# Performance work log

Hardware: AMD Instinct MI355X
Metric: run time of the kernel (lower is better)

## Reference

```python
import jax, jax.numpy as jnp
import numpy as np

N, E, R, H, FDIM, OUT = 50000, 800000, 12, 128, 1582, 2
Q = H // 4  # 32
SLOPE = 0.01  # LeakyReLU default negative slope


def leaky(x):
    return jnp.where(x > 0, x, SLOPE * x)


def rgcn(x, src, dst, etype, W, root, bias):
    # Per-relation mean aggregation of neighbor features, then linear transform
    # (PyG RGCNConv default aggr='mean'). Linear => transform-then-mean is equal.
    # count of edges of each (relation, dst) pair
    seg = etype * N + dst
    cnt = jnp.zeros((R * N,), x.dtype).at[seg].add(1.0)
    norm = 1.0 / jnp.maximum(cnt[seg], 1.0)          # [E]
    xw = jnp.einsum('nh,rhd->nrd', x, W)             # [N,R,H] per-relation transform
    msg = xw[src, etype] * norm[:, None]             # [E,H] gather + normalize
    agg = jax.ops.segment_sum(msg, dst, num_segments=N)  # [N,H] scatter-add
    return agg + x @ root + bias


def setup_inputs() -> dict:
    key = jax.random.key(0)
    ks = jax.random.split(key, 16)
    s = lambda d: 1.0 / np.sqrt(d)
    inp = {
        'feature': jax.random.normal(ks[0], (N, FDIM), jnp.float32),
        'edge_index': jax.random.randint(ks[1], (2, E), 0, N),
        'edge_type': jax.random.randint(ks[2], (E,), 0, R),
        'W_des': jax.random.normal(ks[3], (768, Q), jnp.float32) * s(768),
        'b_des': jnp.zeros((Q,), jnp.float32),
        'W_tweet': jax.random.normal(ks[4], (768, Q), jnp.float32) * s(768),
        'b_tweet': jnp.zeros((Q,), jnp.float32),
        'W_num': jax.random.normal(ks[5], (34, Q), jnp.float32) * s(34),
        'b_num': jnp.zeros((Q,), jnp.float32),
        'W_cat': jax.random.normal(ks[6], (12, Q), jnp.float32) * s(12),
        'b_cat': jnp.zeros((Q,), jnp.float32),
        'W_in': jax.random.normal(ks[7], (H, H), jnp.float32) * s(H),
        'b_in': jnp.zeros((H,), jnp.float32),
        'rgcn_W': jax.random.normal(ks[8], (R, H, H), jnp.float32) * s(H),
        'rgcn_root': jax.random.normal(ks[9], (H, H), jnp.float32) * s(H),
        'rgcn_bias': jnp.zeros((H,), jnp.float32),
        'W_out1': jax.random.normal(ks[10], (H, H), jnp.float32) * s(H),
        'b_out1': jnp.zeros((H,), jnp.float32),
        'W_out2': jax.random.normal(ks[11], (H, OUT), jnp.float32) * s(H),
        'b_out2': jnp.zeros((OUT,), jnp.float32),
    }
    return inp


def reference(feature, edge_index, edge_type, W_des, b_des, W_tweet, b_tweet,
              W_num, b_num, W_cat, b_cat, W_in, b_in, rgcn_W, rgcn_root,
              rgcn_bias, W_out1, b_out1, W_out2, b_out2):
    src, dst = edge_index[0], edge_index[1]
    d = leaky(feature[:, -1536:-768] @ W_des + b_des)
    t = leaky(feature[:, -768:] @ W_tweet + b_tweet)
    num = leaky(feature[:, 12:46] @ W_num + b_num)
    cat = leaky(feature[:, 0:12] @ W_cat + b_cat)
    x = jnp.concatenate((d, t, num, cat), axis=1)       # [N,H]
    x = leaky(x @ W_in + b_in)
    x = rgcn(x, src, dst, edge_type, rgcn_W, rgcn_root, rgcn_bias)
    # dropout: identity in eval mode (deterministic reference)
    x = rgcn(x, src, dst, edge_type, rgcn_W, rgcn_root, rgcn_bias)
    x = leaky(x @ W_out1 + b_out1)
    return x @ W_out2 + b_out2
```

## Files before the change

### kernel.cpp

```cpp
#include <hip/hip_runtime.h>
#include <stdint.h>

#define NN 50000
#define NE 800000
#define NR 12
#define NRX 13
#define NH 128
#define NF 1582
#define NSEG (NN * NR)
#define MT 3125
#define MT2 1563
#define SCAN_NB ((NSEG + 255) / 256)
#define KSENC 50
#define CTXW (NRX * 8)

typedef __attribute__((ext_vector_type(8))) short short8;
typedef __attribute__((ext_vector_type(4))) float floatx4;

__device__ __forceinline__ float bf2f(unsigned int u16) {
    union { unsigned int i; float f; } w; w.i = u16 << 16; return w.f;
}
__device__ __forceinline__ unsigned short f2bf(float f) {
    union { float f; unsigned int i; } w; w.f = f;
    unsigned int i = w.i;
    return (unsigned short)((i + 0x7FFFu + ((i >> 16) & 1u)) >> 16);
}
__device__ __forceinline__ float leaky_f(float v) { return v > 0.f ? v : 0.01f * v; }
__device__ __forceinline__ float fast_rcp(float x) {
    float r; asm("v_rcp_f32 %0, %1" : "=v"(r) : "v"(x)); return r;
}

__global__ __launch_bounds__(256) void swz_k(
    const float* __restrict__ src1, int K1,
    const float* __restrict__ src2, int Ktot, int N, int KS,
    unsigned short* __restrict__ dst)
{
    const int idx = blockIdx.x * 256 + threadIdx.x;
    const int total = (N >> 4) * KS * 512;
    if (idx >= total) return;
    const int j = idx & 7;
    const int lane = (idx >> 3) & 63;
    const int cks = idx >> 9;
    const int ks = cks % KS;
    const int ct = cks / KS;
    const int k = ks * 32 + (lane >> 4) * 8 + j;
    const int col = ct * 16 + (lane & 15);
    float v = 0.f;
    if (k < Ktot) v = (k < K1) ? src1[(size_t)k * N + col] : src2[(size_t)(k - K1) * N + col];
    dst[idx] = f2bf(v);
}

__global__ __launch_bounds__(256) void swzxw_k(
    const float* __restrict__ rgW, const float* __restrict__ root,
    unsigned short* __restrict__ dst)
{
    const int idx = blockIdx.x * 256 + threadIdx.x;
    const int total = CTXW * 4 * 512;
    if (idx >= total) return;
    const int j = idx & 7;
    const int lane = (idx >> 3) & 63;
    const int cks = idx >> 9;
    const int ks = cks & 3;
    const int ctg = cks >> 2;
    const int r = ctg >> 3;
    const int ct8 = ctg & 7;
    const int k = ks * 32 + (lane >> 4) * 8 + j;
    const int c = ct8 * 16 + (lane & 15);
    const float v = (r < NR) ? rgW[((size_t)r * NH + k) * NH + c]
                             : root[(size_t)k * NH + c];
    dst[idx] = f2bf(v);
}

__global__ __launch_bounds__(256) void swzenc_k(
    const float* __restrict__ Wdes, const float* __restrict__ Wtw,
    const float* __restrict__ Wnum, const float* __restrict__ Wcat,
    unsigned short* __restrict__ dst)
{
    const int idx = blockIdx.x * 256 + threadIdx.x;
    const int total = 8 * KSENC * 512;
    if (idx >= total) return;
    const int j = idx & 7;
    const int lane = (idx >> 3) & 63;
    const int cks = idx >> 9;
    const int ks = cks % KSENC;
    const int ct = cks / KSENC;
    const int k = ks * 32 + (lane >> 4) * 8 + j;
    const int col = ct * 16 + (lane & 15);
    float v = 0.f;
    if (col < 32) {
        if (k >= 46 && k < 814)   v = Wdes[(size_t)(k - 46) * 32 + col];
    } else if (col < 64) {
        if (k >= 814 && k < 1582) v = Wtw[(size_t)(k - 814) * 32 + (col - 32)];
    } else if (col < 96) {
        if (k >= 12 && k < 46)    v = Wnum[(size_t)(k - 12) * 32 + (col - 64)];
    } else {
        if (k < 12)               v = Wcat[(size_t)k * 32 + (col - 96)];
    }
    dst[idx] = f2bf(v);
}

__global__ __launch_bounds__(128) void packbias_k(
    const float* __restrict__ bdes, const float* __restrict__ btw,
    const float* __restrict__ bnum, const float* __restrict__ bcat,
    float* __restrict__ be)
{
    const int c = threadIdx.x;
    float v;
    if (c < 32) v = bdes[c];
    else if (c < 64) v = btw[c - 32];
    else if (c < 96) v = bnum[c - 64];
    else v = bcat[c - 96];
    be[c] = v;
}

__global__ __launch_bounds__(256) void hist_k(const int* __restrict__ dst,
                                              const int* __restrict__ et,
                                              int* __restrict__ deg)
{
    const int e = blockIdx.x * 256 + threadIdx.x;
    if (e >= NE) return;
    atomicAdd(&deg[dst[e] * NR + et[e]], 1);
}

__global__ __launch_bounds__(256) void scanA_k(const int* __restrict__ deg,
                                               int* __restrict__ offs,
                                               int* __restrict__ part)
{
    __shared__ int lds[256];
    const int i = blockIdx.x * 256 + threadIdx.x;
    const int v = (i < NSEG) ? deg[i] : 0;
    lds[threadIdx.x] = v; __syncthreads();
#pragma unroll
    for (int d = 1; d < 256; d <<= 1) {
        const int t = (threadIdx.x >= d) ? lds[threadIdx.x - d] : 0;
        __syncthreads();
        lds[threadIdx.x] += t;
        __syncthreads();
    }
    if (i < NSEG) offs[i] = lds[threadIdx.x] - v;
    if (threadIdx.x == 255) part[blockIdx.x] = lds[255];
}

__global__ __launch_bounds__(256) void scanB_k(int* __restrict__ part, int nb)
{
    __shared__ int lds[256];
    __shared__ int carry;
    if (threadIdx.x == 0) carry = 0;
    __syncthreads();
    for (int base = 0; base < nb; base += 256) {
        const int i = base + threadIdx.x;
        const int v = (i < nb) ? part[i] : 0;
        lds[threadIdx.x] = v; __syncthreads();
#pragma unroll
        for (int d = 1; d < 256; d <<= 1) {
            const int t = (threadIdx.x >= d) ? lds[threadIdx.x - d] : 0;
            __syncthreads();
            lds[threadIdx.x] += t;
            __syncthreads();
        }
        if (i < nb) part[i] = lds[threadIdx.x] - v + carry;
        __syncthreads();
        if (threadIdx.x == 255) carry += lds[255];
        __syncthreads();
    }
}

__global__ __launch_bounds__(256) void scanC_k(int* __restrict__ offs,
                                               const int* __restrict__ part)
{
    const int i = blockIdx.x * 256 + threadIdx.x;
    if (i < NSEG) offs[i] += part[blockIdx.x];
}

__global__ __launch_bounds__(256) void fill_k(const int* __restrict__ src,
                                              const int* __restrict__ dst,
                                              const int* __restrict__ et,
                                              const int* __restrict__ offs,
                                              const int* __restrict__ deg,
                                              int* __restrict__ cur,
                                              unsigned int* __restrict__ eidx)
{
    const int e = blockIdx.x * 256 + threadIdx.x;
    if (e >= NE) return;
    const int r = et[e];
    const int s = dst[e] * NR + r;
    const int pos = offs[s] + atomicAdd(&cur[s], 1);
    int n = deg[s]; if (n > 4095) n = 4095;
    eidx[pos] = (unsigned int)(src[e] * NRX + r) | ((unsigned int)n << 20);
}

__global__ __launch_bounds__(256) void enc_k(
    const float* __restrict__ feat,
    const unsigned short* __restrict__ Benc, const float* __restrict__ be,
    const unsigned short* __restrict__ Bwin, const float* __restrict__ bin,
    unsigned short* __restrict__ xa)
{
    const int wave = threadIdx.x >> 6, lane = threadIdx.x & 63;
    const int q = lane >> 4, cl = lane & 15;
    int tile = blockIdx.x * 4 + wave;
    if (tile >= MT) tile = MT - 1;
    const int row = tile * 16 + cl;

    const int lo[8] = {1, 1, 25, 25, 0, 0, 0, 0};
    const int hi[8] = {26, 26, 50, 50, 2, 2, 1, 1};

    floatx4 acc[8];
#pragma unroll
    for (int ct = 0; ct < 8; ct++) { floatx4 z = {0.f,0.f,0.f,0.f}; acc[ct] = z; }

    for (int ks = 0; ks < KSENC; ks++) {
        const int kb = ks * 32 + q * 8;
        union { short8 v; unsigned short u[8]; } a;
        const float* ap = feat + (size_t)row * NF + kb;
        if (kb + 7 < NF) {
#pragma unroll
            for (int j = 0; j < 4; j++) {
                const float2 t = *(const float2*)__builtin_assume_aligned(ap + 2 * j, 8);
                a.u[2 * j]     = f2bf(t.x);
                a.u[2 * j + 1] = f2bf(t.y);
            }
        } else {
#pragma unroll
            for (int j = 0; j < 8; j++)
                a.u[j] = ((kb + j) < NF) ? f2bf(ap[j]) : 0;
        }
#pragma unroll
        for (int ct = 0; ct < 8; ct++) {
            if (ks >= lo[ct] && ks < hi[ct]) {
                const short8 b = *(const short8*)(Benc + ((size_t)(ct * KSENC + ks) * 64 + lane) * 8);
                acc[ct] = __builtin_amdgcn_mfma_f32_16x16x32_bf16(a.v, b, acc[ct], 0, 0, 0);
            }
        }
    }

    __shared__ unsigned short lds[4][16][136];
#pragma unroll
    for (int ct = 0; ct < 8; ct++) {
        const int col = ct * 16 + cl;
        const float bv = be[col];
#pragma unroll
        for (int r = 0; r < 4; r++)
            lds[wave][q * 4 + r][col] = f2bf(leaky_f(acc[ct][r] + bv));
    }
    __syncthreads();

    floatx4 acc2[8];
#pragma unroll
    for (int ct = 0; ct < 8; ct++) { floatx4 z = {0.f,0.f,0.f,0.f}; acc2[ct] = z; }
#pragma unroll
    for (int ks2 = 0; ks2 < 4; ks2++) {
        const short8 a2 = *(const short8*)&lds[wave][cl][ks2 * 32 + q * 8];
#pragma unroll
        for (int ct = 0; ct < 8; ct++) {
            const short8 b = *(const short8*)(Bwin + ((size_t)(ct * 4 + ks2) * 64 + lane) * 8);
            acc2[ct] = __builtin_amdgcn_mfma_f32_16x16x32_bf16(a2, b, acc2[ct], 0, 0, 0);
        }
    }
#pragma unroll
    for (int ct = 0; ct < 8; ct++) {
        const int col = ct * 16 + cl;
        const float bv = bin[col];
#pragma unroll
        for (int r = 0; r < 4; r++)
            xa[(size_t)(tile * 16 + q * 4 + r) * NH + col] = f2bf(leaky_f(acc2[ct][r] + bv));
    }
}

__global__ __launch_bounds__(256) void xw_k(
    const unsigned short* __restrict__ xin,
    const unsigned short* __restrict__ Bxw,
    unsigned short* __restrict__ xw)
{
    const int wave = threadIdx.x >> 6, lane = threadIdx.x & 63;
    const int q = lane >> 4, cl = lane & 15;
    const int wid = blockIdx.x * 4 + wave;
    if (wid >= MT2 * NRX) return;
    const int t2 = wid / NRX;
    const int r = wid - t2 * NRX;
    const int ta = t2 * 2;
    const int tb = (ta + 1 < MT) ? ta + 1 : MT - 1;

    floatx4 accA[8], accB[8];
#pragma unroll
    for (int ct = 0; ct < 8; ct++) {
        floatx4 z = {0.f,0.f,0.f,0.f}; accA[ct] = z; accB[ct] = z;
    }
#pragma unroll
    for (int ks = 0; ks < 4; ks++) {
        const short8 aA = *(const short8*)__builtin_assume_aligned(
            xin + (size_t)(ta * 16 + cl) * NH + ks * 32 + q * 8, 16);
        const short8 aB = *(const short8*)__builtin_assume_aligned(
            xin + (size_t)(tb * 16 + cl) * NH + ks * 32 + q * 8, 16);
#pragma unroll
        for (int ct = 0; ct < 8; ct++) {
            const short8 b = *(const short8*)(Bxw + ((size_t)((r * 8 + ct) * 4 + ks) * 64 + lane) * 8);
            accA[ct] = __builtin_amdgcn_mfma_f32_16x16x32_bf16(aA, b, accA[ct], 0, 0, 0);
            accB[ct] = __builtin_amdgcn_mfma_f32_16x16x32_bf16(aB, b, accB[ct], 0, 0, 0);
        }
    }
#pragma unroll
    for (int ct = 0; ct < 8; ct++) {
        const int col = ct * 16 + cl;
#pragma unroll
        for (int rr = 0; rr < 4; rr++) {
            xw[((size_t)(ta * 16 + q * 4 + rr) * NRX + r) * NH + col] = f2bf(accA[ct][rr]);
            xw[((size_t)(tb * 16 + q * 4 + rr) * NRX + r) * NH + col] = f2bf(accB[ct][rr]);
        }
    }
}

#define ACC8(fk, t, w) \
    fk[0] += (w) * bf2f(t.x & 0xFFFFu); fk[1] += (w) * bf2f(t.x >> 16); \
    fk[2] += (w) * bf2f(t.y & 0xFFFFu); fk[3] += (w) * bf2f(t.y >> 16); \
    fk[4] += (w) * bf2f(t.z & 0xFFFFu); fk[5] += (w) * bf2f(t.z >> 16); \
    fk[6] += (w) * bf2f(t.w & 0xFFFFu); fk[7] += (w) * bf2f(t.w >> 16);

__global__ __launch_bounds__(256) void gather_k(
    const unsigned short* __restrict__ xw,
    const unsigned int* __restrict__ eidx,
    const int* __restrict__ offs,
    const float* __restrict__ rbias,
    unsigned short* __restrict__ xout)
{
    const int wave = threadIdx.x >> 6, lane = threadIdx.x & 63;
    const int q = lane >> 4, cl = lane & 15;
    const int tile = blockIdx.x * 4 + wave;
    if (tile >= MT) return;
    const int d = tile * 16 + cl;
    const int beg = offs[d * NR];
    const int end = (d < NN - 1) ? offs[(d + 1) * NR] : NE;

    float f[4][8];
    {
        const unsigned short* xr = xw + ((size_t)d * NRX + NR) * NH + q * 8;
#pragma unroll
        for (int ki = 0; ki < 4; ki++) {
            const uint4 t = *(const uint4*)(xr + ki * 32);
            f[ki][0] = bf2f(t.x & 0xFFFFu); f[ki][1] = bf2f(t.x >> 16);
            f[ki][2] = bf2f(t.y & 0xFFFFu); f[ki][3] = bf2f(t.y >> 16);
            f[ki][4] = bf2f(t.z & 0xFFFFu); f[ki][5] = bf2f(t.z >> 16);
            f[ki][6] = bf2f(t.w & 0xFFFFu); f[ki][7] = bf2f(t.w >> 16);
        }
    }

    unsigned int vnext = (beg < end) ? eidx[beg] : 0u;
    for (int e = beg; e < end; ++e) {
        const unsigned int val = vnext;
        if (e + 1 < end) vnext = eidx[e + 1];
        const float w = fast_rcp((float)(val >> 20));
        const unsigned short* xr = xw + (size_t)(val & 0xFFFFFu) * NH + q * 8;
        const uint4 t0 = *(const uint4*)(xr);
        const uint4 t1 = *(const uint4*)(xr + 32);
        const uint4 t2 = *(const uint4*)(xr + 64);
        const uint4 t3 = *(const uint4*)(xr + 96);
        ACC8(f[0], t0, w); ACC8(f[1], t1, w); ACC8(f[2], t2, w); ACC8(f[3], t3, w);
    }

#pragma unroll
    for (int ki = 0; ki < 4; ki++) {
        union { short8 v; unsigned short u[8]; } o;
#pragma unroll
        for (int m = 0; m < 8; m++)
            o.u[m] = f2bf(f[ki][m] + rbias[ki * 32 + q * 8 + m]);
        *(short8*)(xout + (size_t)d * NH + ki * 32 + q * 8) = o.v;
    }
}

__global__ __launch_bounds__(256) void head_k(
    const unsigned short* __restrict__ xa,
    const unsigned short* __restrict__ Bo1, const float* __restrict__ bo1,
    const float* __restrict__ Wo2, const float* __restrict__ bo2,
    float* __restrict__ out)
{
    const int wave = threadIdx.x >> 6, lane = threadIdx.x & 63;
    const int q = lane >> 4, cl = lane & 15;
    int tile = blockIdx.x * 4 + wave;
    if (tile >= MT) tile = MT - 1;

    floatx4 acc[8];
#pragma unroll
    for (int ct = 0; ct < 8; ct++) { floatx4 z = {0.f,0.f,0.f,0.f}; acc[ct] = z; }
#pragma unroll
    for (int ks = 0; ks < 4; ks++) {
        const short8 a = *(const short8*)__builtin_assume_aligned(
            xa + (size_t)(tile * 16 + cl) * NH + ks * 32 + q * 8, 16);
#pragma unroll
        for (int ct = 0; ct < 8; ct++) {
            const short8 b = *(const short8*)(Bo1 + ((size_t)(ct * 4 + ks) * 64 + lane) * 8);
            acc[ct] = __builtin_amdgcn_mfma_f32_16x16x32_bf16(a, b, acc[ct], 0, 0, 0);
        }
    }
    __shared__ unsigned short lds[4][16][136];
#pragma unroll
    for (int ct = 0; ct < 8; ct++) {
        const int col = ct * 16 + cl;
        const float bv = bo1[col];
#pragma unroll
        for (int r = 0; r < 4; r++)
            lds[wave][q * 4 + r][col] = f2bf(leaky_f(acc[ct][r] + bv));
    }
    __syncthreads();

    if (lane < 32) {
        const int row = lane >> 1, o = lane & 1;
        float s = bo2[o];
        for (int k = 0; k < NH; k++)
            s += bf2f(lds[wave][row][k]) * Wo2[k * 2 + o];
        out[(size_t)(tile * 16 + row) * 2 + o] = s;
    }
}

extern "C" void kernel_launch(void* const* d_in, const int* in_sizes, int n_in,
                              void* d_out, int out_size, void* d_ws, size_t ws_size,
                              hipStream_t stream)
{
    const float* feat = (const float*)d_in[0];
    const int* ei   = (const int*)d_in[1];
    const int* et   = (const int*)d_in[2];
    const float* Wdes = (const float*)d_in[3];
    const float* bdes = (const float*)d_in[4];
    const float* Wtw  = (const float*)d_in[5];
    const float* btw  = (const float*)d_in[6];
    const float* Wnum = (const float*)d_in[7];
    const float* bnum = (const float*)d_in[8];
    const float* Wcat = (const float*)d_in[9];
    const float* bcat = (const float*)d_in[10];
    const float* Win  = (const float*)d_in[11];
    const float* bin  = (const float*)d_in[12];
    const float* rgW  = (const float*)d_in[13];
    const float* root = (const float*)d_in[14];
    const float* rbias= (const float*)d_in[15];
    const float* Wo1  = (const float*)d_in[16];
    const float* bo1  = (const float*)d_in[17];
    const float* Wo2  = (const float*)d_in[18];
    const float* bo2  = (const float*)d_in[19];
    const int* srcp = ei;
    const int* dstp = ei + NE;

    char* p = (char*)d_ws;
    auto alloc = [&](size_t bytes) { char* r = p; p += (bytes + 255) & ~(size_t)255; return r; };
    unsigned short* xa = (unsigned short*)alloc((size_t)NN * NH * 2);
    unsigned short* xb = (unsigned short*)alloc((size_t)NN * NH * 2);
    int* deg  = (int*)alloc((size_t)NSEG * 4);
    int* offs = (int*)alloc((size_t)NSEG * 4);
    int* cur  = (int*)alloc((size_t)NSEG * 4);
    int* part = (int*)alloc((size_t)(SCAN_NB + 8) * 4);
    unsigned int* eidx = (unsigned int*)alloc((size_t)NE * 4);
    unsigned short* Benc = (unsigned short*)alloc((size_t)8 * KSENC * 512 * 2);
    unsigned short* sWin = (unsigned short*)alloc((size_t)8 * 4 * 512 * 2);
    unsigned short* Bxw  = (unsigned short*)alloc((size_t)CTXW * 4 * 512 * 2);
    unsigned short* sWo1 = (unsigned short*)alloc((size_t)8 * 4 * 512 * 2);
    float* be = (float*)alloc(128 * 4);
    unsigned short* xwbuf = (unsigned short*)alloc((size_t)NN * NRX * NH * 2);

    const int GB = (MT + 3) / 4;
    const int GBXW = (MT2 * NRX + 3) / 4;

    hipMemsetAsync(deg, 0, (size_t)NSEG * 4, stream);
    hipMemsetAsync(cur, 0, (size_t)NSEG * 4, stream);
    hist_k<<<(NE + 255) / 256, 256, 0, stream>>>(dstp, et, deg);
    scanA_k<<<SCAN_NB, 256, 0, stream>>>(deg, offs, part);
    scanB_k<<<1, 256, 0, stream>>>(part, SCAN_NB);
    scanC_k<<<SCAN_NB, 256, 0, stream>>>(offs, part);
    fill_k<<<(NE + 255) / 256, 256, 0, stream>>>(srcp, dstp, et, offs, deg, cur, eidx);

    swzenc_k<<<(8 * KSENC * 512 + 255) / 256, 256, 0, stream>>>(Wdes, Wtw, Wnum, Wcat, Benc);
    packbias_k<<<1, 128, 0, stream>>>(bdes, btw, bnum, bcat, be);
    swz_k<<<(8 * 4 * 512 + 255) / 256, 256, 0, stream>>>(Win, 128, Win, 128, 128, 4, sWin);
    swzxw_k<<<(CTXW * 4 * 512 + 255) / 256, 256, 0, stream>>>(rgW, root, Bxw);
    swz_k<<<(8 * 4 * 512 + 255) / 256, 256, 0, stream>>>(Wo1, 128, Wo1, 128, 128, 4, sWo1);

    enc_k<<<GB, 256, 0, stream>>>(feat, Benc, be, sWin, bin, xa);
    xw_k<<<GBXW, 256, 0, stream>>>(xa, Bxw, xwbuf);
    gather_k<<<GB, 256, 0, stream>>>(xwbuf, eidx, offs, rbias, xb);
    xw_k<<<GBXW, 256, 0, stream>>>(xb, Bxw, xwbuf);
    gather_k<<<GB, 256, 0, stream>>>(xwbuf, eidx, offs, rbias, xa);
    head_k<<<GB, 256, 0, stream>>>(xa, sWo1, bo1, Wo2, bo2, (float*)d_out);
}
```

Baseline: 863.4 us.

## Stage xw output through LDS for coalesced stores; split gather across two waves per tile

The xw kernel now writes each wave's bf16 result tile into shared memory and then emits 16-byte row-contiguous stores, replacing the scattered 2-byte column stores. The out-of-range waves are clamped instead of returning so every thread reaches the block barrier. The gather kernel assigns two waves per 16-node tile, each covering half the feature columns. It also unrolls the edge loop by two so more independent gathers are in flight. This doubles the index and offset reads per node and adds LDS traffic and a block-wide sync in xw.

```diff
diff --git a/kernel.cpp b/kernel.cpp
--- a/kernel.cpp
+++ b/kernel.cpp
@@ -273,8 +273,9 @@
 {
     const int wave = threadIdx.x >> 6, lane = threadIdx.x & 63;
     const int q = lane >> 4, cl = lane & 15;
-    const int wid = blockIdx.x * 4 + wave;
-    if (wid >= MT2 * NRX) return;
+    int wid = blockIdx.x * 4 + wave;
+    if (wid >= MT2 * NRX) wid = MT2 * NRX - 1;
+    __shared__ unsigned short tl[4][2][16][136];
     const int t2 = wid / NRX;
     const int r = wid - t2 * NRX;
     const int ta = t2 * 2;
@@ -303,17 +304,32 @@
         const int col = ct * 16 + cl;
 #pragma unroll
         for (int rr = 0; rr < 4; rr++) {
-            xw[((size_t)(ta * 16 + q * 4 + rr) * NRX + r) * NH + col] = f2bf(accA[ct][rr]);
-            xw[((size_t)(tb * 16 + q * 4 + rr) * NRX + r) * NH + col] = f2bf(accB[ct][rr]);
-        }
-    }
-}
-
-#define ACC8(fk, t, w) \
-    fk[0] += (w) * bf2f(t.x & 0xFFFFu); fk[1] += (w) * bf2f(t.x >> 16); \
-    fk[2] += (w) * bf2f(t.y & 0xFFFFu); fk[3] += (w) * bf2f(t.y >> 16); \
-    fk[4] += (w) * bf2f(t.z & 0xFFFFu); fk[5] += (w) * bf2f(t.z >> 16); \
-    fk[6] += (w) * bf2f(t.w & 0xFFFFu); fk[7] += (w) * bf2f(t.w >> 16);
+            tl[wave][0][q * 4 + rr][col] = f2bf(accA[ct][rr]);
+            tl[wave][1][q * 4 + rr][col] = f2bf(accB[ct][rr]);
+        }
+    }
+    __syncthreads();
+#pragma unroll
+    for (int i = 0; i < 4; i++) {
+        const int row = i * 4 + q;
+        const short8 vA = *(const short8*)&tl[wave][0][row][cl * 8];
+        const short8 vB = *(const short8*)&tl[wave][1][row][cl * 8];
+        *(short8*)(xw + ((size_t)(ta * 16 + row) * NRX + r) * NH + cl * 8) = vA;
+        *(short8*)(xw + ((size_t)(tb * 16 + row) * NRX + r) * NH + cl * 8) = vB;
+    }
+}
+
+#define ACC8(fk, tv, wv) \
+    fk[0] += (wv) * bf2f((tv).x & 0xFFFFu); fk[1] += (wv) * bf2f((tv).x >> 16); \
+    fk[2] += (wv) * bf2f((tv).y & 0xFFFFu); fk[3] += (wv) * bf2f((tv).y >> 16); \
+    fk[4] += (wv) * bf2f((tv).z & 0xFFFFu); fk[5] += (wv) * bf2f((tv).z >> 16); \
+    fk[6] += (wv) * bf2f((tv).w & 0xFFFFu); fk[7] += (wv) * bf2f((tv).w >> 16);
+
+#define INIT8(fk, tv) \
+    fk[0] = bf2f((tv).x & 0xFFFFu); fk[1] = bf2f((tv).x >> 16); \
+    fk[2] = bf2f((tv).y & 0xFFFFu); fk[3] = bf2f((tv).y >> 16); \
+    fk[4] = bf2f((tv).z & 0xFFFFu); fk[5] = bf2f((tv).z >> 16); \
+    fk[6] = bf2f((tv).w & 0xFFFFu); fk[7] = bf2f((tv).w >> 16);
 
 __global__ __launch_bounds__(256) void gather_k(
     const unsigned short* __restrict__ xw,
@@ -324,46 +340,48 @@
 {
     const int wave = threadIdx.x >> 6, lane = threadIdx.x & 63;
     const int q = lane >> 4, cl = lane & 15;
-    const int tile = blockIdx.x * 4 + wave;
+    const int wid = blockIdx.x * 4 + wave;
+    const int tile = wid >> 1;
     if (tile >= MT) return;
+    const int half = wid & 1;
+    const int cA = half * 8 + q;
+    const int cB = cA + 4;
     const int d = tile * 16 + cl;
     const int beg = offs[d * NR];
     const int end = (d < NN - 1) ? offs[(d + 1) * NR] : NE;
 
-    float f[4][8];
+    float fA[8], fB[8];
     {
-        const unsigned short* xr = xw + ((size_t)d * NRX + NR) * NH + q * 8;
-#pragma unroll
-        for (int ki = 0; ki < 4; ki++) {
-            const uint4 t = *(const uint4*)(xr + ki * 32);
-            f[ki][0] = bf2f(t.x & 0xFFFFu); f[ki][1] = bf2f(t.x >> 16);
-            f[ki][2] = bf2f(t.y & 0xFFFFu); f[ki][3] = bf2f(t.y >> 16);
-            f[ki][4] = bf2f(t.z & 0xFFFFu); f[ki][5] = bf2f(t.z >> 16);
-            f[ki][6] = bf2f(t.w & 0xFFFFu); f[ki][7] = bf2f(t.w >> 16);
-        }
-    }
-
-    unsigned int vnext = (beg < end) ? eidx[beg] : 0u;
-    for (int e = beg; e < end; ++e) {
-        const unsigned int val = vnext;
-        if (e + 1 < end) vnext = eidx[e + 1];
-        const float w = fast_rcp((float)(val >> 20));
-        const unsigned short* xr = xw + (size_t)(val & 0xFFFFFu) * NH + q * 8;
-        const uint4 t0 = *(const uint4*)(xr);
-        const uint4 t1 = *(const uint4*)(xr + 32);
-        const uint4 t2 = *(const uint4*)(xr + 64);
-        const uint4 t3 = *(const uint4*)(xr + 96);
-        ACC8(f[0], t0, w); ACC8(f[1], t1, w); ACC8(f[2], t2, w); ACC8(f[3], t3, w);
-    }
-
-#pragma unroll
-    for (int ki = 0; ki < 4; ki++) {
-        union { short8 v; unsigned short u[8]; } o;
-#pragma unroll
-        for (int m = 0; m < 8; m++)
-            o.u[m] = f2bf(f[ki][m] + rbias[ki * 32 + q * 8 + m]);
-        *(short8*)(xout + (size_t)d * NH + ki * 32 + q * 8) = o.v;
-    }
+        const unsigned short* xr = xw + ((size_t)d * NRX + NR) * NH;
+        const uint4 tA = *(const uint4*)(xr + cA * 8);
+        const uint4 tB = *(const uint4*)(xr + cB * 8);
+        INIT8(fA, tA); INIT8(fB, tB);
+    }
+
+    for (int e = beg; e < end; e += 2) {
+        const int e1 = (e + 1 < end) ? e + 1 : e;
+        const unsigned int v0 = eidx[e];
+        const unsigned int v1 = eidx[e1];
+        const float w0 = fast_rcp((float)(v0 >> 20));
+        const float w1 = (e + 1 < end) ? fast_rcp((float)(v1 >> 20)) : 0.f;
+        const unsigned short* x0 = xw + (size_t)(v0 & 0xFFFFFu) * NH;
+        const unsigned short* x1 = xw + (size_t)(v1 & 0xFFFFFu) * NH;
+        const uint4 a0 = *(const uint4*)(x0 + cA * 8);
+        const uint4 b0 = *(const uint4*)(x0 + cB * 8);
+        const uint4 a1 = *(const uint4*)(x1 + cA * 8);
+        const uint4 b1 = *(const uint4*)(x1 + cB * 8);
+        ACC8(fA, a0, w0); ACC8(fB, b0, w0);
+        ACC8(fA, a1, w1); ACC8(fB, b1, w1);
+    }
+
+    union { short8 v; unsigned short u[8]; } oA, oB;
+#pragma unroll
+    for (int m = 0; m < 8; m++) {
+        oA.u[m] = f2bf(fA[m] + rbias[cA * 8 + m]);
+        oB.u[m] = f2bf(fB[m] + rbias[cB * 8 + m]);
+    }
+    *(short8*)(xout + (size_t)d * NH + cA * 8) = oA.v;
+    *(short8*)(xout + (size_t)d * NH + cB * 8) = oB.v;
 }
 
 __global__ __launch_bounds__(256) void head_k(
@@ -455,6 +473,7 @@
 
     const int GB = (MT + 3) / 4;
     const int GBXW = (MT2 * NRX + 3) / 4;
+    const int GB2 = (MT * 2 + 3) / 4;
 
     hipMemsetAsync(deg, 0, (size_t)NSEG * 4, stream);
     hipMemsetAsync(cur, 0, (size_t)NSEG * 4, stream);
@@ -472,8 +491,8 @@
 
     enc_k<<<GB, 256, 0, stream>>>(feat, Benc, be, sWin, bin, xa);
     xw_k<<<GBXW, 256, 0, stream>>>(xa, Bxw, xwbuf);
-    gather_k<<<GB, 256, 0, stream>>>(xwbuf, eidx, offs, rbias, xb);
+    gather_k<<<GB2, 256, 0, stream>>>(xwbuf, eidx, offs, rbias, xb);
     xw_k<<<GBXW, 256, 0, stream>>>(xb, Bxw, xwbuf);
-    gather_k<<<GB, 256, 0, stream>>>(xwbuf, eidx, offs, rbias, xa);
+    gather_k<<<GB2, 256, 0, stream>>>(xwbuf, eidx, offs, rbias, xa);
     head_k<<<GB, 256, 0, stream>>>(xa, sWo1, bo1, Wo2, bo2, (float*)d_out);
 }
```

Measured after the change: 840.9 us. 2.6% less time.
